# Kernel optimization log

Measured on AMD Instinct MI355X. Metric: run time of the kernel, lower is better.

## Reference

```python
import jax, jax.numpy as jnp
import numpy as np

B, T, ENC_DIM, QUERY_DIM = 128, 1024, 512, 1024
ATT_DIM, ATT_FILTERS, ATT_KERNEL = 128, 32, 31


def setup_inputs() -> dict:
    key = jax.random.key(0)
    ks = jax.random.split(key, 9)
    inv = lambda d: 1.0 / np.sqrt(d)
    return {
        "query": jax.random.normal(ks[0], (B, QUERY_DIM), jnp.float32),
        "memory": jax.random.normal(ks[1], (B, T, ENC_DIM), jnp.float32),
        "processed_memory": jax.random.normal(ks[2], (B, T, ATT_DIM), jnp.float32),
        "attention_weights_cat": jax.random.uniform(ks[3], (B, T, 2), jnp.float32),
        # learned params
        "W_query": jax.random.normal(ks[4], (QUERY_DIM, ATT_DIM), jnp.float32) * inv(QUERY_DIM),
        "conv_kernel": jax.random.normal(ks[5], (ATT_KERNEL, 2, ATT_FILTERS), jnp.float32) * inv(ATT_KERNEL * 2),
        "W_loc": jax.random.normal(ks[6], (ATT_FILTERS, ATT_DIM), jnp.float32) * inv(ATT_FILTERS),
        "v": jax.random.normal(ks[7], (ATT_DIM, 1), jnp.float32) * inv(ATT_DIM),
    }


def reference(query, memory, processed_memory, attention_weights_cat,
              W_query, conv_kernel, W_loc, v):
    # processed_query: (B, 1, A)
    pq = (query @ W_query)[:, None, :]
    # location features: Conv1D same-padding, no bias, channels-last -> (B, T, F) -> (B, T, A)
    loc = jax.lax.conv_general_dilated(
        attention_weights_cat, conv_kernel,
        window_strides=(1,), padding="SAME",
        dimension_numbers=("NWC", "WIO", "NWC"))
    loc = loc @ W_loc
    # additive energies: (B, T)
    energies = jnp.squeeze(jnp.tanh(pq + loc + processed_memory) @ v, axis=-1)
    attention_weights = jax.nn.softmax(energies, axis=1)
    # context: (B, ENC_DIM)
    attention_context = jnp.einsum("bt,btd->bd", attention_weights, memory)
    return attention_context, attention_weights
```

## Files before the change

kernel.cpp:

```cpp
#include <hip/hip_runtime.h>
#include <hip/hip_bf16.h>

#define BB 128
#define TT 1024
#define ENC_DIM 512
#define QUERY_DIM 1024
#define ATT_DIM 128
#define ATT_FILTERS 32
#define ATT_KERNEL 31
#define TILE_T 64
#define NTILE (TT / TILE_T)

using f32x4 = __attribute__((ext_vector_type(4))) float;
using f32x2 = __attribute__((ext_vector_type(2))) float;

__device__ __forceinline__ float tanh_fast(float x) {
    float e = __expf(2.0f * x);
    return 1.0f - 2.0f * __builtin_amdgcn_rcpf(1.0f + e);
}

__global__ __launch_bounds__(256) void k_pq(const float* __restrict__ query,
                                            const float* __restrict__ Wq,
                                            float* __restrict__ pqp) {
    __shared__ float q[512];
    __shared__ float pp[128];
    int b = blockIdx.x, h = blockIdx.y;
    int tid = threadIdx.x, a = tid & 127, ks = tid >> 7;
    for (int i = tid; i < 512; i += 256) q[i] = query[b * QUERY_DIM + h * 512 + i];
    __syncthreads();
    const float* w  = Wq + (h * 512 + ks * 256) * ATT_DIM + a;
    const float* qs = q + ks * 256;
    float acc = 0.f;
#pragma unroll 16
    for (int k = 0; k < 256; ++k) acc += qs[k] * w[k * ATT_DIM];
    if (ks) pp[a] = acc;
    __syncthreads();
    if (!ks) pqp[(h * BB + b) * ATT_DIM + a] = acc + pp[a];
}

__global__ __launch_bounds__(256, 4) void k_fused(
    const float* __restrict__ aw,
    const float* __restrict__ ck,
    const float* __restrict__ Wloc,
    const float* __restrict__ pm,
    const float* __restrict__ pqp,
    const float* __restrict__ v,
    const float* __restrict__ mem,
    float* __restrict__ energies,
    float* __restrict__ partP,
    float* __restrict__ partS)
{
    __shared__ float s_aw[(TILE_T + 30) * 2];
    __shared__ float s_ck[ATT_KERNEL * 2 * ATT_FILTERS];
    __shared__ float s_f[TILE_T * ATT_FILTERS];
    __shared__ float s_e[TILE_T];
    __shared__ float s_w[TILE_T];
    __shared__ f32x4 sr[ENC_DIM / 4];

    int s = blockIdx.x, b = blockIdx.y;
    int t0 = s * TILE_T;
    int tid = threadIdx.x;

    for (int i = tid; i < ATT_KERNEL * 2 * ATT_FILTERS; i += 256) s_ck[i] = ck[i];
    for (int i = tid; i < (TILE_T + 30) * 2; i += 256) {
        int ii = i >> 1, c = i & 1;
        int t = t0 - 15 + ii;
        s_aw[i] = (t >= 0 && t < TT) ? aw[(b * TT + t) * 2 + c] : 0.f;
    }
    __syncthreads();

    {
        int j = tid & 31;
        float wk0[ATT_KERNEL], wk1[ATT_KERNEL];
#pragma unroll
        for (int k = 0; k < ATT_KERNEL; ++k) {
            wk0[k] = s_ck[k * 64 + j];
            wk1[k] = s_ck[k * 64 + 32 + j];
        }
        for (int t = tid >> 5; t < TILE_T; t += 8) {
            float acc0 = 0.f, acc1 = 0.f;
#pragma unroll
            for (int k = 0; k < ATT_KERNEL; ++k) {
                float2 awp = *reinterpret_cast<const float2*>(&s_aw[(t + k) * 2]);
                acc0 += awp.x * wk0[k];
                acc1 += awp.y * wk1[k];
            }
            s_f[t * ATT_FILTERS + j] = acc0 + acc1;
        }
    }
    __syncthreads();

    {
        int w = tid >> 6, lane = tid & 63;
        int a = lane * 2;
        float2 wl[ATT_FILTERS];
#pragma unroll
        for (int j = 0; j < ATT_FILTERS; ++j)
            wl[j] = *reinterpret_cast<const float2*>(&Wloc[j * ATT_DIM + a]);
        float2 pqA = *reinterpret_cast<const float2*>(&pqp[b * ATT_DIM + a]);
        float2 pqB = *reinterpret_cast<const float2*>(&pqp[(BB + b) * ATT_DIM + a]);
        float pq0 = pqA.x + pqB.x, pq1 = pqA.y + pqB.y;
        float2 vv = *reinterpret_cast<const float2*>(&v[a]);
        const float* pmb = pm + ((long)(b * TT + t0)) * ATT_DIM + a;

        auto process = [&](int t, float2 c) {
            float x0 = pq0 + c.x;
            float x1 = pq1 + c.y;
            const float4* f4 = reinterpret_cast<const float4*>(&s_f[t * ATT_FILTERS]);
#pragma unroll
            for (int j4 = 0; j4 < ATT_FILTERS / 4; ++j4) {
                float4 f = f4[j4];
                x0 += f.x * wl[4 * j4].x     + f.y * wl[4 * j4 + 1].x
                    + f.z * wl[4 * j4 + 2].x + f.w * wl[4 * j4 + 3].x;
                x1 += f.x * wl[4 * j4].y     + f.y * wl[4 * j4 + 1].y
                    + f.z * wl[4 * j4 + 2].y + f.w * wl[4 * j4 + 3].y;
            }
            float e = tanh_fast(x0) * vv.x + tanh_fast(x1) * vv.y;
#pragma unroll
            for (int off = 32; off > 0; off >>= 1) e += __shfl_xor(e, off);
            if (lane == 0) {
                s_e[t] = e;
                energies[b * TT + t0 + t] = e;
            }
        };

#pragma unroll
        for (int g = 0; g < 4; ++g) {
            int tg = w + g * 16;
            float2 c0 = *reinterpret_cast<const float2*>(&pmb[(tg)      * ATT_DIM]);
            float2 c1 = *reinterpret_cast<const float2*>(&pmb[(tg + 4)  * ATT_DIM]);
            float2 c2 = *reinterpret_cast<const float2*>(&pmb[(tg + 8)  * ATT_DIM]);
            float2 c3 = *reinterpret_cast<const float2*>(&pmb[(tg + 12) * ATT_DIM]);
            process(tg, c0);
            process(tg + 4, c1);
            process(tg + 8, c2);
            process(tg + 12, c3);
        }
    }
    __syncthreads();

    float ex = 0.f;
    if (tid < TILE_T) {
        ex = __expf(s_e[tid]);
        s_w[tid] = ex;
    }
    __syncthreads();
    if (tid < 64) {
        float ss = ex;
#pragma unroll
        for (int off = 32; off > 0; off >>= 1) ss += __shfl_xor(ss, off);
        if (tid == 0) partS[s * BB + b] = ss;
    }

    int p = tid >> 7, q = tid & 127;
    const f32x4* m4 = reinterpret_cast<const f32x4*>(mem + ((long)(b * TT + t0)) * ENC_DIM) + q;
    f32x4 acc = {0.f, 0.f, 0.f, 0.f};
#pragma unroll 16
    for (int t = p; t < TILE_T; t += 2) {
        float wt = s_w[t];
        f32x4 mv = __builtin_nontemporal_load(&m4[(long)t * (ENC_DIM / 4)]);
        acc += wt * mv;
    }
    __syncthreads();
    if (p == 1) sr[q] = acc;
    __syncthreads();
    if (p == 0) {
        acc += sr[q];
        reinterpret_cast<f32x4*>(partP)[(s * BB + b) * (ENC_DIM / 4) + q] = acc;
    }
}

__global__ __launch_bounds__(256) void k_final(
    const float* __restrict__ energies,
    const float* __restrict__ partP,
    const float* __restrict__ partS,
    float* __restrict__ wts,
    float* __restrict__ ctx)
{
    int b = blockIdx.x;
    int tid = threadIdx.x;

    float S = 0.f;
#pragma unroll
    for (int i = 0; i < NTILE; ++i) S += partS[i * BB + b];
    float invS = 1.0f / S;

    {
        float4 e = reinterpret_cast<const float4*>(energies + b * TT)[tid];
        float4 w;
        w.x = __expf(e.x) * invS;
        w.y = __expf(e.y) * invS;
        w.z = __expf(e.z) * invS;
        w.w = __expf(e.w) * invS;
        reinterpret_cast<float4*>(wts + b * TT)[tid] = w;
    }
    {
        f32x2 acc2 = {0.f, 0.f};
#pragma unroll
        for (int i = 0; i < NTILE; ++i) {
            f32x2 pv = *reinterpret_cast<const f32x2*>(&partP[((long)(i * BB + b)) * ENC_DIM + 2 * tid]);
            acc2 += pv;
        }
        acc2 *= invS;
        *reinterpret_cast<f32x2*>(&ctx[b * ENC_DIM + 2 * tid]) = acc2;
    }
}

extern "C" void kernel_launch(void* const* d_in, const int* in_sizes, int n_in,
                              void* d_out, int out_size, void* d_ws, size_t ws_size,
                              hipStream_t stream) {
    const float* query  = (const float*)d_in[0];
    const float* memory = (const float*)d_in[1];
    const float* pm     = (const float*)d_in[2];
    const float* awc    = (const float*)d_in[3];
    const float* Wq     = (const float*)d_in[4];
    const float* ck     = (const float*)d_in[5];
    const float* Wloc   = (const float*)d_in[6];
    const float* v      = (const float*)d_in[7];

    float* out = (float*)d_out;
    float* ctx = out;
    float* wts = out + BB * ENC_DIM;

    float* pqp      = (float*)d_ws;
    float* energies = pqp + 2 * BB * ATT_DIM;
    float* partP    = energies + BB * TT;
    float* partS    = partP + (long)NTILE * BB * ENC_DIM;

    k_pq   <<<dim3(BB, 2),     dim3(256), 0, stream>>>(query, Wq, pqp);
    k_fused<<<dim3(NTILE, BB), dim3(256), 0, stream>>>(awc, ck, Wloc, pm, pqp, v,
                                                       memory, energies, partP, partS);
    k_final<<<dim3(BB),        dim3(256), 0, stream>>>(energies, partP, partS, wts, ctx);
}
```

Baseline: 88.02 us.

## Process two time tiles per block, overlapping energy compute with memory reduction

Each block now handles two 64-step tiles. While waves 0-1 compute the energies for the second tile, waves 2-3 stream memory and accumulate the weighted context for the first tile, so the compute-heavy and bandwidth-heavy phases run side by side. The exp and per-wave partial sums now happen inside the energy routine, which removes a separate exp/reduce phase and its barriers. The cost is half as many blocks (1024 instead of 2048), an unbalanced split of work across waves, and more partial sums for the final kernel to read.

```diff
diff --git a/kernel.cpp b/kernel.cpp
--- a/kernel.cpp
+++ b/kernel.cpp
@@ -9,7 +9,8 @@
 #define ATT_FILTERS 32
 #define ATT_KERNEL 31
 #define TILE_T 64
-#define NTILE (TT / TILE_T)
+#define PAIRS 8
+#define NCHUNK 16
 
 using f32x4 = __attribute__((ext_vector_type(4))) float;
 using f32x2 = __attribute__((ext_vector_type(2))) float;
@@ -50,19 +51,18 @@
     float* __restrict__ partP,
     float* __restrict__ partS)
 {
-    __shared__ float s_aw[(TILE_T + 30) * 2];
+    __shared__ float s_aw[(2 * TILE_T + 30) * 2];
     __shared__ float s_ck[ATT_KERNEL * 2 * ATT_FILTERS];
-    __shared__ float s_f[TILE_T * ATT_FILTERS];
-    __shared__ float s_e[TILE_T];
-    __shared__ float s_w[TILE_T];
+    __shared__ float s_f[2 * TILE_T * ATT_FILTERS];
+    __shared__ float s_w[2 * TILE_T];
     __shared__ f32x4 sr[ENC_DIM / 4];
 
-    int s = blockIdx.x, b = blockIdx.y;
-    int t0 = s * TILE_T;
+    int px = blockIdx.x, b = blockIdx.y;
+    int t0 = px * 2 * TILE_T;
     int tid = threadIdx.x;
 
     for (int i = tid; i < ATT_KERNEL * 2 * ATT_FILTERS; i += 256) s_ck[i] = ck[i];
-    for (int i = tid; i < (TILE_T + 30) * 2; i += 256) {
+    for (int i = tid; i < (2 * TILE_T + 30) * 2; i += 256) {
         int ii = i >> 1, c = i & 1;
         int t = t0 - 15 + ii;
         s_aw[i] = (t >= 0 && t < TT) ? aw[(b * TT + t) * 2 + c] : 0.f;
@@ -77,7 +77,7 @@
             wk0[k] = s_ck[k * 64 + j];
             wk1[k] = s_ck[k * 64 + 32 + j];
         }
-        for (int t = tid >> 5; t < TILE_T; t += 8) {
+        for (int t = tid >> 5; t < 2 * TILE_T; t += 8) {
             float acc0 = 0.f, acc1 = 0.f;
 #pragma unroll
             for (int k = 0; k < ATT_KERNEL; ++k) {
@@ -90,40 +90,43 @@
     }
     __syncthreads();
 
-    {
-        int w = tid >> 6, lane = tid & 63;
-        int a = lane * 2;
-        float2 wl[ATT_FILTERS];
-#pragma unroll
-        for (int j = 0; j < ATT_FILTERS; ++j)
-            wl[j] = *reinterpret_cast<const float2*>(&Wloc[j * ATT_DIM + a]);
-        float2 pqA = *reinterpret_cast<const float2*>(&pqp[b * ATT_DIM + a]);
-        float2 pqB = *reinterpret_cast<const float2*>(&pqp[(BB + b) * ATT_DIM + a]);
-        float pq0 = pqA.x + pqB.x, pq1 = pqA.y + pqB.y;
-        float2 vv = *reinterpret_cast<const float2*>(&v[a]);
-        const float* pmb = pm + ((long)(b * TT + t0)) * ATT_DIM + a;
-
-        auto process = [&](int t, float2 c) {
-            float x0 = pq0 + c.x;
-            float x1 = pq1 + c.y;
-            const float4* f4 = reinterpret_cast<const float4*>(&s_f[t * ATT_FILTERS]);
-#pragma unroll
-            for (int j4 = 0; j4 < ATT_FILTERS / 4; ++j4) {
-                float4 f = f4[j4];
-                x0 += f.x * wl[4 * j4].x     + f.y * wl[4 * j4 + 1].x
-                    + f.z * wl[4 * j4 + 2].x + f.w * wl[4 * j4 + 3].x;
-                x1 += f.x * wl[4 * j4].y     + f.y * wl[4 * j4 + 1].y
-                    + f.z * wl[4 * j4 + 2].y + f.w * wl[4 * j4 + 3].y;
-            }
-            float e = tanh_fast(x0) * vv.x + tanh_fast(x1) * vv.y;
-#pragma unroll
-            for (int off = 32; off > 0; off >>= 1) e += __shfl_xor(e, off);
-            if (lane == 0) {
-                s_e[t] = e;
-                energies[b * TT + t0 + t] = e;
-            }
-        };
-
+    int w = tid >> 6, lane = tid & 63;
+    int a = lane * 2;
+    float2 wl[ATT_FILTERS];
+#pragma unroll
+    for (int j = 0; j < ATT_FILTERS; ++j)
+        wl[j] = *reinterpret_cast<const float2*>(&Wloc[j * ATT_DIM + a]);
+    float2 pqA = *reinterpret_cast<const float2*>(&pqp[b * ATT_DIM + a]);
+    float2 pqB = *reinterpret_cast<const float2*>(&pqp[(BB + b) * ATT_DIM + a]);
+    float pq0 = pqA.x + pqB.x, pq1 = pqA.y + pqB.y;
+    float2 vv = *reinterpret_cast<const float2*>(&v[a]);
+    const float* pmb = pm + ((long)(b * TT + t0)) * ATT_DIM + a;
+
+    auto process = [&](int t, float2 c) -> float {
+        float x0 = pq0 + c.x;
+        float x1 = pq1 + c.y;
+        const float4* f4 = reinterpret_cast<const float4*>(&s_f[t * ATT_FILTERS]);
+#pragma unroll
+        for (int j4 = 0; j4 < ATT_FILTERS / 4; ++j4) {
+            float4 f = f4[j4];
+            x0 += f.x * wl[4 * j4].x     + f.y * wl[4 * j4 + 1].x
+                + f.z * wl[4 * j4 + 2].x + f.w * wl[4 * j4 + 3].x;
+            x1 += f.x * wl[4 * j4].y     + f.y * wl[4 * j4 + 1].y
+                + f.z * wl[4 * j4 + 2].y + f.w * wl[4 * j4 + 3].y;
+        }
+        float e = tanh_fast(x0) * vv.x + tanh_fast(x1) * vv.y;
+#pragma unroll
+        for (int off = 32; off > 0; off >>= 1) e += __shfl_xor(e, off);
+        float ex = __expf(e);
+        if (lane == 0) {
+            s_w[t] = ex;
+            energies[b * TT + t0 + t] = e;
+        }
+        return ex;
+    };
+
+    {
+        float sumexp = 0.f;
 #pragma unroll
         for (int g = 0; g < 4; ++g) {
             int tg = w + g * 16;
@@ -131,42 +134,61 @@
             float2 c1 = *reinterpret_cast<const float2*>(&pmb[(tg + 4)  * ATT_DIM]);
             float2 c2 = *reinterpret_cast<const float2*>(&pmb[(tg + 8)  * ATT_DIM]);
             float2 c3 = *reinterpret_cast<const float2*>(&pmb[(tg + 12) * ATT_DIM]);
-            process(tg, c0);
-            process(tg + 4, c1);
-            process(tg + 8, c2);
-            process(tg + 12, c3);
-        }
-    }
-    __syncthreads();
-
-    float ex = 0.f;
-    if (tid < TILE_T) {
-        ex = __expf(s_e[tid]);
-        s_w[tid] = ex;
-    }
-    __syncthreads();
-    if (tid < 64) {
-        float ss = ex;
-#pragma unroll
-        for (int off = 32; off > 0; off >>= 1) ss += __shfl_xor(ss, off);
-        if (tid == 0) partS[s * BB + b] = ss;
-    }
-
-    int p = tid >> 7, q = tid & 127;
-    const f32x4* m4 = reinterpret_cast<const f32x4*>(mem + ((long)(b * TT + t0)) * ENC_DIM) + q;
-    f32x4 acc = {0.f, 0.f, 0.f, 0.f};
+            sumexp += process(tg, c0);
+            sumexp += process(tg + 4, c1);
+            sumexp += process(tg + 8, c2);
+            sumexp += process(tg + 12, c3);
+        }
+        if (lane == 0) partS[(px * 6 + w) * BB + b] = sumexp;
+    }
+    __syncthreads();
+
+    if (tid < 128) {
+        float sumexp1 = 0.f;
+#pragma unroll
+        for (int g = 0; g < 8; ++g) {
+            int tg = 64 + w + g * 8;
+            float2 c0 = *reinterpret_cast<const float2*>(&pmb[(tg)     * ATT_DIM]);
+            float2 c1 = *reinterpret_cast<const float2*>(&pmb[(tg + 2) * ATT_DIM]);
+            float2 c2 = *reinterpret_cast<const float2*>(&pmb[(tg + 4) * ATT_DIM]);
+            float2 c3 = *reinterpret_cast<const float2*>(&pmb[(tg + 6) * ATT_DIM]);
+            sumexp1 += process(tg, c0);
+            sumexp1 += process(tg + 2, c1);
+            sumexp1 += process(tg + 4, c2);
+            sumexp1 += process(tg + 6, c3);
+        }
+        if (lane == 0) partS[(px * 6 + 4 + w) * BB + b] = sumexp1;
+    } else {
+        int q = tid & 127;
+        const f32x4* m4 = reinterpret_cast<const f32x4*>(mem + ((long)(b * TT + t0)) * ENC_DIM) + q;
+        f32x4 acc = {0.f, 0.f, 0.f, 0.f};
 #pragma unroll 16
-    for (int t = p; t < TILE_T; t += 2) {
-        float wt = s_w[t];
-        f32x4 mv = __builtin_nontemporal_load(&m4[(long)t * (ENC_DIM / 4)]);
-        acc += wt * mv;
-    }
-    __syncthreads();
-    if (p == 1) sr[q] = acc;
-    __syncthreads();
-    if (p == 0) {
-        acc += sr[q];
-        reinterpret_cast<f32x4*>(partP)[(s * BB + b) * (ENC_DIM / 4) + q] = acc;
+        for (int t = 0; t < TILE_T; ++t) {
+            float wt = s_w[t];
+            f32x4 mv = __builtin_nontemporal_load(&m4[(long)t * (ENC_DIM / 4)]);
+            acc += wt * mv;
+        }
+        reinterpret_cast<f32x4*>(partP)[((2 * px) * BB + b) * (ENC_DIM / 4) + q] = acc;
+    }
+    __syncthreads();
+
+    {
+        int p = tid >> 7, q = tid & 127;
+        const f32x4* m4 = reinterpret_cast<const f32x4*>(mem + ((long)(b * TT + t0 + TILE_T)) * ENC_DIM) + q;
+        f32x4 acc = {0.f, 0.f, 0.f, 0.f};
+#pragma unroll 16
+        for (int t = p; t < TILE_T; t += 2) {
+            float wt = s_w[TILE_T + t];
+            f32x4 mv = __builtin_nontemporal_load(&m4[(long)t * (ENC_DIM / 4)]);
+            acc += wt * mv;
+        }
+        __syncthreads();
+        if (p == 1) sr[q] = acc;
+        __syncthreads();
+        if (p == 0) {
+            acc += sr[q];
+            reinterpret_cast<f32x4*>(partP)[((2 * px + 1) * BB + b) * (ENC_DIM / 4) + q] = acc;
+        }
     }
 }
 
@@ -182,7 +204,7 @@
 
     float S = 0.f;
 #pragma unroll
-    for (int i = 0; i < NTILE; ++i) S += partS[i * BB + b];
+    for (int i = 0; i < PAIRS * 6; ++i) S += partS[i * BB + b];
     float invS = 1.0f / S;
 
     {
@@ -197,7 +219,7 @@
     {
         f32x2 acc2 = {0.f, 0.f};
 #pragma unroll
-        for (int i = 0; i < NTILE; ++i) {
+        for (int i = 0; i < NCHUNK; ++i) {
             f32x2 pv = *reinterpret_cast<const f32x2*>(&partP[((long)(i * BB + b)) * ENC_DIM + 2 * tid]);
             acc2 += pv;
         }
@@ -225,10 +247,10 @@
     float* pqp      = (float*)d_ws;
     float* energies = pqp + 2 * BB * ATT_DIM;
     float* partP    = energies + BB * TT;
-    float* partS    = partP + (long)NTILE * BB * ENC_DIM;
+    float* partS    = partP + (long)NCHUNK * BB * ENC_DIM;
 
     k_pq   <<<dim3(BB, 2),     dim3(256), 0, stream>>>(query, Wq, pqp);
-    k_fused<<<dim3(NTILE, BB), dim3(256), 0, stream>>>(awc, ck, Wloc, pm, pqp, v,
+    k_fused<<<dim3(PAIRS, BB), dim3(256), 0, stream>>>(awc, ck, Wloc, pm, pqp, v,
                                                        memory, energies, partP, partS);
     k_final<<<dim3(BB),        dim3(256), 0, stream>>>(energies, partP, partS, wts, ctx);
 }
```

Result: slower. 109.1 us (+23.9%).
